# Kernel tuning notes

Measured on AMD Instinct MI355X. Metric: run time of the kernel, lower is better.

## Reference

```python
import jax, jax.numpy as jnp
import numpy as np

B, S, C, V, LAT, NL = 256, 512, 256, 32, 256, 7
DILS = [1, 2, 4, 8, 16, 32, 64]
EPS = 1e-5


def setup_inputs() -> dict:
    key = jax.random.key(0)
    ks = jax.random.split(key, 24)
    s = 0.05
    inp = {
        "x": jax.random.randint(ks[0], (B, S), 0, V, dtype=jnp.int64 if jax.config.read("jax_enable_x64") else jnp.int32),
        "z": jax.random.normal(ks[1], (B, LAT), dtype=jnp.float32),
        "emb": jax.random.normal(ks[2], (V, C), dtype=jnp.float32) * s,
        "latent_W": jax.random.normal(ks[3], (LAT, C), dtype=jnp.float32) * s,
        "latent_b": jnp.zeros((C,), jnp.float32),
        "ln1_g": jnp.ones((NL, C), jnp.float32),
        "ln1_b": jnp.zeros((NL, C), jnp.float32),
        "w1": jax.random.normal(ks[4], (NL, C, C), jnp.float32) * s,
        "b1": jnp.zeros((NL, C), jnp.float32),
        "ln2_g": jnp.ones((NL, C), jnp.float32),
        "ln2_b": jnp.zeros((NL, C), jnp.float32),
        "wd": jax.random.normal(ks[5], (NL, 2, C, C), jnp.float32) * s,  # tap 0 = x[t-d], tap 1 = x[t]
        "bd": jnp.zeros((NL, C), jnp.float32),
        "ln3_g": jnp.ones((NL, C), jnp.float32),
        "ln3_b": jnp.zeros((NL, C), jnp.float32),
        "we": jax.random.normal(ks[6], (NL, C, C), jnp.float32) * s,
        "be": jnp.zeros((NL, C), jnp.float32),
        "wg": jax.random.normal(ks[7], (NL, C, C), jnp.float32) * s,
        "bg": jnp.zeros((NL, C), jnp.float32),
        "out_W": jax.random.normal(ks[8], (C, V), jnp.float32) * s,
        "out_b": jnp.zeros((V,), jnp.float32),
    }
    return inp


def _ln(h, g, b):
    mu = h.mean(-1, keepdims=True)
    var = jnp.mean((h - mu) ** 2, axis=-1, keepdims=True)
    return (h - mu) * jax.lax.rsqrt(var + EPS) * g + b


def _lrelu(h):
    return jnp.where(h >= 0, h, 0.01 * h)


def reference(x, z, emb, latent_W, latent_b, ln1_g, ln1_b, w1, b1,
              ln2_g, ln2_b, wd, bd, ln3_g, ln3_b, we, be, wg, bg,
              out_W, out_b):
    # channel-last layout [B, S, C] throughout (fuses away the torch transposes)
    h = emb[x] + (z @ latent_W + latent_b)[:, None, :]
    for i, d in enumerate(DILS):
        x_inp = h
        t = _lrelu(_ln(x_inp, ln1_g[i], ln1_b[i]))
        t = t @ w1[i] + b1[i]
        t = _lrelu(_ln(t, ln2_g[i], ln2_b[i]))
        # causal dilated conv, kernel=2: out[t] = W0*x[t-d] + W1*x[t]
        t_shift = jnp.pad(t, ((0, 0), (d, 0), (0, 0)))[:, :t.shape[1], :]
        t = t_shift @ wd[i, 0] + t @ wd[i, 1] + bd[i]
        t = _lrelu(_ln(t, ln3_g[i], ln3_b[i]))
        gated = (t @ we[i] + be[i]) * jax.nn.sigmoid(t @ wg[i] + bg[i])
        h = gated + x_inp
    logits = h @ out_W + out_b                      # [B, S, V]
    lp = jax.nn.log_softmax(logits, axis=-1)
    # gather log-prob of next token: lp[:, :-1, :] at x[:, 1:]
    return jnp.take_along_axis(lp[:, :-1, :], x[:, 1:, None], axis=2)[..., 0]
```

## Files before the change

### kernel.cpp

```cpp
#include <hip/hip_runtime.h>

typedef unsigned short u16;
typedef unsigned int   u32;
typedef __attribute__((ext_vector_type(8))) short short8;
typedef __attribute__((ext_vector_type(4))) float f32x4;

struct __align__(8) u16x4 { u16 x, y, z, w; };

#define NL 7
#define M_DIM 131072

__device__ __forceinline__ float b2f(u16 u) {
  union { float f; u32 i; } c; c.i = ((u32)u) << 16; return c.f;
}
__device__ __forceinline__ u16 f2b(float f) {
  union { float f; u32 i; } c; c.f = f;
  u32 r = c.i + 0x7FFFu + ((c.i >> 16) & 1u);
  return (u16)(r >> 16);
}
__device__ __forceinline__ float wave_sum(float v) {
  #pragma unroll
  for (int off = 1; off < 64; off <<= 1) v += __shfl_xor(v, off);
  return v;
}
__device__ __forceinline__ void gload16(const void* g, void* l) {
  __builtin_amdgcn_global_load_lds((const __attribute__((address_space(1))) void*)g,
                                   (__attribute__((address_space(3))) void*)l, 16, 0, 0);
}


__global__ __launch_bounds__(256) void conv_w1_k(const float* __restrict__ w1, u16* __restrict__ wT) {
  int idx = blockIdx.x * 256 + threadIdx.x;
  int i = idx >> 16, rem = idx & 65535;
  int n = rem >> 8, k = rem & 255;
  wT[idx] = f2b(w1[(i << 16) + (k << 8) + n]);
}

__global__ __launch_bounds__(256) void conv_wd_k(const float* __restrict__ wd, u16* __restrict__ wT) {
  int idx = blockIdx.x * 256 + threadIdx.x;
  int i = idx / 131072, rem = idx & 131071;
  int n = rem >> 9, k2 = rem & 511;
  int tap = k2 >> 8, k = k2 & 255;
  wT[idx] = f2b(wd[(((i * 2 + tap) << 8) + k) * 256 + n]);
}

__global__ __launch_bounds__(256) void conv_weg_k(const float* __restrict__ we, const float* __restrict__ wg,
                                                  u16* __restrict__ wT) {
  int idx = blockIdx.x * 256 + threadIdx.x;
  int i = idx / 131072, rem = idx & 131071;
  int src = rem >> 16, n = (rem >> 8) & 255, k = rem & 255;
  const float* W = src ? wg : we;
  wT[idx] = f2b(W[((i << 8) + k) * 256 + n]);
}

__global__ __launch_bounds__(256) void conv_wo_k(const float* __restrict__ outW, u16* __restrict__ wTo) {
  int idx = blockIdx.x * 256 + threadIdx.x;
  int v = idx >> 8, k = idx & 255;
  wTo[idx] = f2b(outW[k * 32 + v]);
}


__global__ __launch_bounds__(256) void zlat_k(const float* __restrict__ z, const float* __restrict__ W,
                                              const float* __restrict__ bias, float* __restrict__ zlat) {
  int b = blockIdx.x, c = threadIdx.x;
  float acc = bias[c];
  for (int l = 0; l < 256; ++l) acc += z[b * 256 + l] * W[l * 256 + c];
  zlat[b * 256 + c] = acc;
}


__device__ __forceinline__ void ln_lrelu4(float v0, float v1, float v2, float v3,
                                          const float* __restrict__ g, const float* __restrict__ b,
                                          int c, u16x4* out) {
  float s = wave_sum(v0 + v1 + v2 + v3);
  float q = wave_sum(v0 * v0 + v1 * v1 + v2 * v2 + v3 * v3);
  float mu = s * 0.00390625f;
  float var = q * 0.00390625f - mu * mu;
  float rs = rsqrtf(var + 1e-5f);
  float4 gv = *(const float4*)&g[c];
  float4 bv = *(const float4*)&b[c];
  float y0 = (v0 - mu) * rs * gv.x + bv.x; y0 = y0 >= 0.f ? y0 : 0.01f * y0;
  float y1 = (v1 - mu) * rs * gv.y + bv.y; y1 = y1 >= 0.f ? y1 : 0.01f * y1;
  float y2 = (v2 - mu) * rs * gv.z + bv.z; y2 = y2 >= 0.f ? y2 : 0.01f * y2;
  float y3 = (v3 - mu) * rs * gv.w + bv.w; y3 = y3 >= 0.f ? y3 : 0.01f * y3;
  out->x = f2b(y0); out->y = f2b(y1); out->z = f2b(y2); out->w = f2b(y3);
}


__global__ __launch_bounds__(256) void embed_ln_k(const int* __restrict__ x, const float* __restrict__ emb,
                                                  const float* __restrict__ zlat,
                                                  const float* __restrict__ g, const float* __restrict__ b,
                                                  u16* __restrict__ h, u16* __restrict__ tOut) {
  int wave = threadIdx.x >> 6, lane = threadIdx.x & 63;
  int r = blockIdx.x * 4 + wave;
  int c = lane * 4;
  int tok = x[r];
  int bi = r >> 9;
  float4 ev = *(const float4*)&emb[tok * 256 + c];
  float4 zv = *(const float4*)&zlat[bi * 256 + c];
  float v0 = ev.x + zv.x, v1 = ev.y + zv.y, v2 = ev.z + zv.z, v3 = ev.w + zv.w;
  u16x4 hb; hb.x = f2b(v0); hb.y = f2b(v1); hb.z = f2b(v2); hb.w = f2b(v3);
  *(u16x4*)&h[(long)r * 256 + c] = hb;
  u16x4 ov;
  ln_lrelu4(v0, v1, v2, v3, g, b, c, &ov);
  *(u16x4*)&tOut[(long)r * 256 + c] = ov;
}


__global__ __launch_bounds__(256) void gemm_ln_k(
    const u16* __restrict__ A, const u16* __restrict__ WT, int Ktot, int dil,
    const float* __restrict__ bias, const float* __restrict__ g, const float* __restrict__ b,
    u16* __restrict__ Out)
{
  __shared__ u16 lA[64 * 32];
  __shared__ u16 lB[256 * 32];
  __shared__ float pS[64][4], pQ[64][4];
  __shared__ float muA[64], rsA[64];
  const int tid = threadIdx.x;
  const int lane = tid & 63;
  const int wv = tid >> 6;
  const int wc = wv * 64;
  const int m0 = blockIdx.x * 64;
  const int rA = tid >> 2;
  const int cA = (tid & 3) * 8;
  const int mm = m0 + rA;
  const int s1 = mm & 511;
  const bool fixBlk = (dil > 0) && ((m0 & 511) < dil);

  f32x4 acc[4][4];
  #pragma unroll
  for (int i = 0; i < 4; ++i)
    #pragma unroll
    for (int j = 0; j < 4; ++j) {
      acc[i][j][0] = 0.f; acc[i][j][1] = 0.f; acc[i][j][2] = 0.f; acc[i][j][3] = 0.f;
    }

  const int nkt = Ktot >> 5;
  for (int kt = 0; kt < nkt; ++kt) {
    const int kk = (kt & 7) * 32;
    int r = mm;
    if (dil > 0 && kt < 8) r = (s1 >= dil) ? (mm - dil) : mm;
    gload16(A + (long)r * 256 + kk + cA, &lA[rA * 32 + cA]);
    const u16* bSrc = WT + (long)rA * Ktot + kt * 32 + cA;
    #pragma unroll
    for (int j = 0; j < 4; ++j)
      gload16(bSrc + (long)(64 * j) * Ktot, &lB[(rA + 64 * j) * 32 + cA]);
    __syncthreads();

    if (fixBlk && kt < 8) {
      if (rA < dil) {
        uint4 zz; zz.x = 0; zz.y = 0; zz.z = 0; zz.w = 0;
        *(uint4*)&lA[rA * 32 + cA] = zz;
      }
      __syncthreads();
    }

    const int lq = (lane >> 4) * 8;
    const int lr = lane & 15;
    short8 af[4], bfr[4];
    #pragma unroll
    for (int mt = 0; mt < 4; ++mt)
      af[mt] = *(const short8*)&lA[(mt * 16 + lr) * 32 + lq];
    #pragma unroll
    for (int nt = 0; nt < 4; ++nt)
      bfr[nt] = *(const short8*)&lB[(wc + nt * 16 + lr) * 32 + lq];
    #pragma unroll
    for (int mt = 0; mt < 4; ++mt)
      #pragma unroll
      for (int nt = 0; nt < 4; ++nt)
        acc[mt][nt] = __builtin_amdgcn_mfma_f32_16x16x32_bf16(af[mt], bfr[nt], acc[mt][nt], 0, 0, 0);
    __syncthreads();
  }

  const int lr = lane & 15;
  const int quad = lane >> 4;
  float biasv[4], gv[4], bv[4];
  #pragma unroll
  for (int nt = 0; nt < 4; ++nt) {
    int n = wc + nt * 16 + lr;
    biasv[nt] = bias[n]; gv[nt] = g[n]; bv[nt] = b[n];
  }
  #pragma unroll
  for (int mt = 0; mt < 4; ++mt)
    #pragma unroll
    for (int r = 0; r < 4; ++r) {
      float s = 0.f, q = 0.f;
      #pragma unroll
      for (int nt = 0; nt < 4; ++nt) {
        float v = acc[mt][nt][r] + biasv[nt];
        acc[mt][nt][r] = v;
        s += v; q += v * v;
      }
      #pragma unroll
      for (int off = 1; off < 16; off <<= 1) {
        s += __shfl_xor(s, off); q += __shfl_xor(q, off);
      }
      if (lr == 0) { pS[mt * 16 + quad * 4 + r][wv] = s; pQ[mt * 16 + quad * 4 + r][wv] = q; }
    }
  __syncthreads();
  if (tid < 64) {
    float S = pS[tid][0] + pS[tid][1] + pS[tid][2] + pS[tid][3];
    float Q = pQ[tid][0] + pQ[tid][1] + pQ[tid][2] + pQ[tid][3];
    float mu = S * 0.00390625f;
    float var = Q * 0.00390625f - mu * mu;
    muA[tid] = mu; rsA[tid] = rsqrtf(var + 1e-5f);
  }
  __syncthreads();
  #pragma unroll
  for (int mt = 0; mt < 4; ++mt)
    #pragma unroll
    for (int r = 0; r < 4; ++r) {
      int row = mt * 16 + quad * 4 + r;
      float mu = muA[row], rs = rsA[row];
      #pragma unroll
      for (int nt = 0; nt < 4; ++nt) {
        float y = (acc[mt][nt][r] - mu) * rs * gv[nt] + bv[nt];
        y = y >= 0.f ? y : 0.01f * y;
        Out[(long)(m0 + row) * 256 + wc + nt * 16 + lr] = f2b(y);
      }
    }
}


__global__ __launch_bounds__(256, 2) void gemm_gate_ln_k(
    const u16* __restrict__ P, const u16* __restrict__ WTe, const u16* __restrict__ WTg,
    const float* __restrict__ be, const float* __restrict__ bg,
    const float* __restrict__ g, const float* __restrict__ b,
    u16* __restrict__ h, u16* __restrict__ tOut, int doLN)
{
  __shared__ u16 lA[64 * 32];
  __shared__ u16 lBe[256 * 32];
  __shared__ u16 lBg[256 * 32];
  __shared__ float pS[64][4], pQ[64][4];
  __shared__ float muA[64], rsA[64];
  const int tid = threadIdx.x;
  const int lane = tid & 63;
  const int wv = tid >> 6;
  const int wc = wv * 64;
  const int m0 = blockIdx.x * 64;
  const int rA = tid >> 2;
  const int cA = (tid & 3) * 8;

  f32x4 accE[4][4], accG[4][4];
  #pragma unroll
  for (int i = 0; i < 4; ++i)
    #pragma unroll
    for (int j = 0; j < 4; ++j) {
      accE[i][j][0] = 0.f; accE[i][j][1] = 0.f; accE[i][j][2] = 0.f; accE[i][j][3] = 0.f;
      accG[i][j][0] = 0.f; accG[i][j][1] = 0.f; accG[i][j][2] = 0.f; accG[i][j][3] = 0.f;
    }

  for (int kt = 0; kt < 8; ++kt) {
    const int kk = kt * 32;
    gload16(P + (long)(m0 + rA) * 256 + kk + cA, &lA[rA * 32 + cA]);
    const long bofs = (long)rA * 256 + kk + cA;
    #pragma unroll
    for (int j = 0; j < 4; ++j) {
      gload16(WTe + bofs + (long)(64 * j) * 256, &lBe[(rA + 64 * j) * 32 + cA]);
      gload16(WTg + bofs + (long)(64 * j) * 256, &lBg[(rA + 64 * j) * 32 + cA]);
    }
    __syncthreads();

    const int lq = (lane >> 4) * 8;
    const int lr = lane & 15;
    short8 af[4], bfe[4], bfg[4];
    #pragma unroll
    for (int mt = 0; mt < 4; ++mt)
      af[mt] = *(const short8*)&lA[(mt * 16 + lr) * 32 + lq];
    #pragma unroll
    for (int nt = 0; nt < 4; ++nt) {
      bfe[nt] = *(const short8*)&lBe[(wc + nt * 16 + lr) * 32 + lq];
      bfg[nt] = *(const short8*)&lBg[(wc + nt * 16 + lr) * 32 + lq];
    }
    #pragma unroll
    for (int mt = 0; mt < 4; ++mt)
      #pragma unroll
      for (int nt = 0; nt < 4; ++nt) {
        accE[mt][nt] = __builtin_amdgcn_mfma_f32_16x16x32_bf16(af[mt], bfe[nt], accE[mt][nt], 0, 0, 0);
        accG[mt][nt] = __builtin_amdgcn_mfma_f32_16x16x32_bf16(af[mt], bfg[nt], accG[mt][nt], 0, 0, 0);
      }
    __syncthreads();
  }

  const int lr = lane & 15;
  const int quad = lane >> 4;
  float bev[4], bgv[4];
  #pragma unroll
  for (int nt = 0; nt < 4; ++nt) {
    int n = wc + nt * 16 + lr;
    bev[nt] = be[n]; bgv[nt] = bg[n];
  }
  #pragma unroll
  for (int mt = 0; mt < 4; ++mt)
    #pragma unroll
    for (int r = 0; r < 4; ++r) {
      int row = mt * 16 + quad * 4 + r;
      long off = (long)(m0 + row) * 256;
      float s = 0.f, q = 0.f;
      #pragma unroll
      for (int nt = 0; nt < 4; ++nt) {
        int n = wc + nt * 16 + lr;
        float e = accE[mt][nt][r] + bev[nt];
        float gg = accG[mt][nt][r] + bgv[nt];
        float hv = b2f(h[off + n]);
        float hn = e * (1.f / (1.f + expf(-gg))) + hv;
        h[off + n] = f2b(hn);
        accE[mt][nt][r] = hn;
        s += hn; q += hn * hn;
      }
      #pragma unroll
      for (int off2 = 1; off2 < 16; off2 <<= 1) {
        s += __shfl_xor(s, off2); q += __shfl_xor(q, off2);
      }
      if (lr == 0) { pS[row][wv] = s; pQ[row][wv] = q; }
    }
  __syncthreads();
  if (tid < 64) {
    float S = pS[tid][0] + pS[tid][1] + pS[tid][2] + pS[tid][3];
    float Q = pQ[tid][0] + pQ[tid][1] + pQ[tid][2] + pQ[tid][3];
    float mu = S * 0.00390625f;
    float var = Q * 0.00390625f - mu * mu;
    muA[tid] = mu; rsA[tid] = rsqrtf(var + 1e-5f);
  }
  __syncthreads();
  if (doLN) {
    float gv[4], bv[4];
    #pragma unroll
    for (int nt = 0; nt < 4; ++nt) {
      int n = wc + nt * 16 + lr;
      gv[nt] = g[n]; bv[nt] = b[n];
    }
    #pragma unroll
    for (int mt = 0; mt < 4; ++mt)
      #pragma unroll
      for (int r = 0; r < 4; ++r) {
        int row = mt * 16 + quad * 4 + r;
        float mu = muA[row], rs = rsA[row];
        #pragma unroll
        for (int nt = 0; nt < 4; ++nt) {
          float y = (accE[mt][nt][r] - mu) * rs * gv[nt] + bv[nt];
          y = y >= 0.f ? y : 0.01f * y;
          tOut[(long)(m0 + row) * 256 + wc + nt * 16 + lr] = f2b(y);
        }
      }
  }
}


__global__ __launch_bounds__(256) void final_k(const u16* __restrict__ h, const u16* __restrict__ WTo,
                                               const float* __restrict__ outb, const int* __restrict__ x,
                                               float* __restrict__ out) {
  __shared__ u16 lW[32 * 264];
  const int tid = threadIdx.x;
  const int lane = tid & 63;
  const int wv = tid >> 6;
  const int mBase = blockIdx.x * 256 + wv * 64;

  #pragma unroll
  for (int j = 0; j < 4; ++j) {
    int chunk = tid + 256 * j;
    int v = chunk >> 5, k8 = chunk & 31;
    uint4 w4 = *(const uint4*)(WTo + v * 256 + k8 * 8);
    *(uint4*)&lW[v * 264 + k8 * 8] = w4;
  }
  __syncthreads();

  const int lq = (lane >> 4) * 8;
  const int lr = lane & 15;
  const int quad = lane >> 4;

  f32x4 acc[4][2];
  #pragma unroll
  for (int mt = 0; mt < 4; ++mt) {
    acc[mt][0][0] = 0.f; acc[mt][0][1] = 0.f; acc[mt][0][2] = 0.f; acc[mt][0][3] = 0.f;
    acc[mt][1][0] = 0.f; acc[mt][1][1] = 0.f; acc[mt][1][2] = 0.f; acc[mt][1][3] = 0.f;
  }

  for (int kt = 0; kt < 8; ++kt) {
    short8 bf0 = *(const short8*)&lW[lr * 264 + kt * 32 + lq];
    short8 bf1 = *(const short8*)&lW[(16 + lr) * 264 + kt * 32 + lq];
    #pragma unroll
    for (int mt = 0; mt < 4; ++mt) {
      short8 af = *(const short8*)(h + (long)(mBase + mt * 16 + lr) * 256 + kt * 32 + lq);
      acc[mt][0] = __builtin_amdgcn_mfma_f32_16x16x32_bf16(af, bf0, acc[mt][0], 0, 0, 0);
      acc[mt][1] = __builtin_amdgcn_mfma_f32_16x16x32_bf16(af, bf1, acc[mt][1], 0, 0, 0);
    }
  }

  float ob0 = outb[lr], ob1 = outb[16 + lr];
  #pragma unroll
  for (int mt = 0; mt < 4; ++mt)
    #pragma unroll
    for (int r = 0; r < 4; ++r) {
      int row = mBase + mt * 16 + quad * 4 + r;
      float lo = acc[mt][0][r] + ob0;
      float hi = acc[mt][1][r] + ob1;
      float mx = fmaxf(lo, hi);
      #pragma unroll
      for (int o = 1; o < 16; o <<= 1) mx = fmaxf(mx, __shfl_xor(mx, o));
      float se = expf(lo - mx) + expf(hi - mx);
      #pragma unroll
      for (int o = 1; o < 16; o <<= 1) se += __shfl_xor(se, o);
      int s = row & 511;
      int xa = (s == 511) ? row : (row + 1);
      int tok = x[xa];
      float lg = (tok < 16) ? lo : hi;
      float lp = lg - mx - logf(se);
      if (s != 511 && lr == (tok & 15))
        out[(row >> 9) * 511 + s] = lp;
    }
}


extern "C" void kernel_launch(void* const* d_in, const int* in_sizes, int n_in,
                              void* d_out, int out_size, void* d_ws, size_t ws_size,
                              hipStream_t stream) {
  const int*   x    = (const int*)d_in[0];
  const float* z    = (const float*)d_in[1];
  const float* emb  = (const float*)d_in[2];
  const float* latW = (const float*)d_in[3];
  const float* latb = (const float*)d_in[4];
  const float* ln1g = (const float*)d_in[5];
  const float* ln1b = (const float*)d_in[6];
  const float* w1   = (const float*)d_in[7];
  const float* b1   = (const float*)d_in[8];
  const float* ln2g = (const float*)d_in[9];
  const float* ln2b = (const float*)d_in[10];
  const float* wd   = (const float*)d_in[11];
  const float* bd   = (const float*)d_in[12];
  const float* ln3g = (const float*)d_in[13];
  const float* ln3b = (const float*)d_in[14];
  const float* we   = (const float*)d_in[15];
  const float* be   = (const float*)d_in[16];
  const float* wg   = (const float*)d_in[17];
  const float* bg   = (const float*)d_in[18];
  const float* outW = (const float*)d_in[19];
  const float* outb = (const float*)d_in[20];

  char* ws = (char*)d_ws;
  u16*   h    = (u16*)(ws + 0);
  u16*   bufA = (u16*)(ws + 67108864);
  u16*   bufB = (u16*)(ws + 134217728);
  float* zlat = (float*)(ws + 201326592);
  u16*   wT1  = (u16*)(ws + 201588736);
  u16*   wTd  = (u16*)(ws + 202506240);
  u16*   wTeg = (u16*)(ws + 204341248);
  u16*   wTo  = (u16*)(ws + 206176256);

  conv_w1_k <<<1792, 256, 0, stream>>>(w1, wT1);
  conv_wd_k <<<3584, 256, 0, stream>>>(wd, wTd);
  conv_weg_k<<<3584, 256, 0, stream>>>(we, wg, wTeg);
  conv_wo_k <<<32, 256, 0, stream>>>(outW, wTo);
  zlat_k    <<<256, 256, 0, stream>>>(z, latW, latb, zlat);
  embed_ln_k<<<M_DIM / 4, 256, 0, stream>>>(x, emb, zlat, ln1g, ln1b, h, bufA);

  u16* X = bufA;
  u16* Y = bufB;
  for (int i = 0; i < NL; ++i) {
    int d = 1 << i;
    int doLN = (i < NL - 1) ? 1 : 0;
    int ni = doLN ? (i + 1) : i;
    gemm_ln_k<<<M_DIM / 64, 256, 0, stream>>>(
        X, wT1 + i * 65536, 256, 0, b1 + i * 256, ln2g + i * 256, ln2b + i * 256, Y);
    gemm_ln_k<<<M_DIM / 64, 256, 0, stream>>>(
        Y, wTd + i * 131072, 512, d, bd + i * 256, ln3g + i * 256, ln3b + i * 256, X);
    gemm_gate_ln_k<<<M_DIM / 64, 256, 0, stream>>>(
        X, wTeg + i * 131072, wTeg + i * 131072 + 65536, be + i * 256, bg + i * 256,
        ln1g + ni * 256, ln1b + ni * 256, h, Y, doLN);
    u16* tmp = X; X = Y; Y = tmp;
  }

  final_k<<<M_DIM / 256, 256, 0, stream>>>(h, wTo, outb, x, (float*)d_out);
}
```

Baseline: 1.693 ms.

## Move LN1 into first GEMM prologue and restage weights through registers

```diff
diff --git a/kernel.cpp b/kernel.cpp
--- a/kernel.cpp
+++ b/kernel.cpp
@@ -17,15 +17,6 @@
   union { float f; u32 i; } c; c.f = f;
   u32 r = c.i + 0x7FFFu + ((c.i >> 16) & 1u);
   return (u16)(r >> 16);
-}
-__device__ __forceinline__ float wave_sum(float v) {
-  #pragma unroll
-  for (int off = 1; off < 64; off <<= 1) v += __shfl_xor(v, off);
-  return v;
-}
-__device__ __forceinline__ void gload16(const void* g, void* l) {
-  __builtin_amdgcn_global_load_lds((const __attribute__((address_space(1))) void*)g,
-                                   (__attribute__((address_space(3))) void*)l, 16, 0, 0);
 }
 
 
@@ -69,28 +60,8 @@
 }
 
 
-__device__ __forceinline__ void ln_lrelu4(float v0, float v1, float v2, float v3,
-                                          const float* __restrict__ g, const float* __restrict__ b,
-                                          int c, u16x4* out) {
-  float s = wave_sum(v0 + v1 + v2 + v3);
-  float q = wave_sum(v0 * v0 + v1 * v1 + v2 * v2 + v3 * v3);
-  float mu = s * 0.00390625f;
-  float var = q * 0.00390625f - mu * mu;
-  float rs = rsqrtf(var + 1e-5f);
-  float4 gv = *(const float4*)&g[c];
-  float4 bv = *(const float4*)&b[c];
-  float y0 = (v0 - mu) * rs * gv.x + bv.x; y0 = y0 >= 0.f ? y0 : 0.01f * y0;
-  float y1 = (v1 - mu) * rs * gv.y + bv.y; y1 = y1 >= 0.f ? y1 : 0.01f * y1;
-  float y2 = (v2 - mu) * rs * gv.z + bv.z; y2 = y2 >= 0.f ? y2 : 0.01f * y2;
-  float y3 = (v3 - mu) * rs * gv.w + bv.w; y3 = y3 >= 0.f ? y3 : 0.01f * y3;
-  out->x = f2b(y0); out->y = f2b(y1); out->z = f2b(y2); out->w = f2b(y3);
-}
-
-
-__global__ __launch_bounds__(256) void embed_ln_k(const int* __restrict__ x, const float* __restrict__ emb,
-                                                  const float* __restrict__ zlat,
-                                                  const float* __restrict__ g, const float* __restrict__ b,
-                                                  u16* __restrict__ h, u16* __restrict__ tOut) {
+__global__ __launch_bounds__(256) void embed_k(const int* __restrict__ x, const float* __restrict__ emb,
+                                               const float* __restrict__ zlat, u16* __restrict__ h) {
   int wave = threadIdx.x >> 6, lane = threadIdx.x & 63;
   int r = blockIdx.x * 4 + wave;
   int c = lane * 4;
@@ -98,34 +69,62 @@
   int bi = r >> 9;
   float4 ev = *(const float4*)&emb[tok * 256 + c];
   float4 zv = *(const float4*)&zlat[bi * 256 + c];
-  float v0 = ev.x + zv.x, v1 = ev.y + zv.y, v2 = ev.z + zv.z, v3 = ev.w + zv.w;
-  u16x4 hb; hb.x = f2b(v0); hb.y = f2b(v1); hb.z = f2b(v2); hb.w = f2b(v3);
+  u16x4 hb;
+  hb.x = f2b(ev.x + zv.x); hb.y = f2b(ev.y + zv.y);
+  hb.z = f2b(ev.z + zv.z); hb.w = f2b(ev.w + zv.w);
   *(u16x4*)&h[(long)r * 256 + c] = hb;
-  u16x4 ov;
-  ln_lrelu4(v0, v1, v2, v3, g, b, c, &ov);
-  *(u16x4*)&tOut[(long)r * 256 + c] = ov;
-}
-
-
-__global__ __launch_bounds__(256) void gemm_ln_k(
-    const u16* __restrict__ A, const u16* __restrict__ WT, int Ktot, int dil,
-    const float* __restrict__ bias, const float* __restrict__ g, const float* __restrict__ b,
-    u16* __restrict__ Out)
+}
+
+
+__global__ __launch_bounds__(256) void gemm1_k(
+    const u16* __restrict__ h, const u16* __restrict__ WT,
+    const float* __restrict__ lnAg, const float* __restrict__ lnAb,
+    const float* __restrict__ bias,
+    const float* __restrict__ lnBg, const float* __restrict__ lnBb,
+    u16* __restrict__ V)
 {
-  __shared__ u16 lA[64 * 32];
-  __shared__ u16 lB[256 * 32];
-  __shared__ float pS[64][4], pQ[64][4];
-  __shared__ float muA[64], rsA[64];
+  __shared__ __align__(16) u16 sm[64 * 264 + 256 * 40];
+  u16* lA = sm;
+  u16* lB = sm + 64 * 264;
   const int tid = threadIdx.x;
   const int lane = tid & 63;
   const int wv = tid >> 6;
   const int wc = wv * 64;
   const int m0 = blockIdx.x * 64;
-  const int rA = tid >> 2;
-  const int cA = (tid & 3) * 8;
-  const int mm = m0 + rA;
-  const int s1 = mm & 511;
-  const bool fixBlk = (dil > 0) && ((m0 & 511) < dil);
+  const int lr = lane & 15;
+  const int quad = lane >> 4;
+  const int lq = quad * 8;
+  const int rB = tid >> 2;
+  const int cB = tid & 3;
+
+  uint4 bq0 = *(const uint4*)(WT + (long)rB * 256 + cB * 8);
+  uint4 bq1 = *(const uint4*)(WT + (long)(rB + 64) * 256 + cB * 8);
+  uint4 bq2 = *(const uint4*)(WT + (long)(rB + 128) * 256 + cB * 8);
+  uint4 bq3 = *(const uint4*)(WT + (long)(rB + 192) * 256 + cB * 8);
+
+  {
+    float4 gv = *(const float4*)&lnAg[lane * 4];
+    float4 bv = *(const float4*)&lnAb[lane * 4];
+    #pragma unroll 4
+    for (int it = 0; it < 16; ++it) {
+      int row = wv * 16 + it;
+      u16x4 hv = *(const u16x4*)&h[(long)(m0 + row) * 256 + lane * 4];
+      float v0 = b2f(hv.x), v1 = b2f(hv.y), v2 = b2f(hv.z), v3 = b2f(hv.w);
+      float s = v0 + v1 + v2 + v3;
+      float q = v0 * v0 + v1 * v1 + v2 * v2 + v3 * v3;
+      #pragma unroll
+      for (int o = 1; o < 64; o <<= 1) { s += __shfl_xor(s, o); q += __shfl_xor(q, o); }
+      float mu = s * 0.00390625f;
+      float var = q * 0.00390625f - mu * mu;
+      float rs = rsqrtf(var + 1e-5f);
+      float y0 = (v0 - mu) * rs * gv.x + bv.x; y0 = y0 >= 0.f ? y0 : 0.01f * y0;
+      float y1 = (v1 - mu) * rs * gv.y + bv.y; y1 = y1 >= 0.f ? y1 : 0.01f * y1;
+      float y2 = (v2 - mu) * rs * gv.z + bv.z; y2 = y2 >= 0.f ? y2 : 0.01f * y2;
+      float y3 = (v3 - mu) * rs * gv.w + bv.w; y3 = y3 >= 0.f ? y3 : 0.01f * y3;
+      u16x4 ov; ov.x = f2b(y0); ov.y = f2b(y1); ov.z = f2b(y2); ov.w = f2b(y3);
+      *(u16x4*)&lA[row * 264 + lane * 4] = ov;
+    }
+  }
 
   f32x4 acc[4][4];
   #pragma unroll
@@ -135,50 +134,45 @@
       acc[i][j][0] = 0.f; acc[i][j][1] = 0.f; acc[i][j][2] = 0.f; acc[i][j][3] = 0.f;
     }
 
-  const int nkt = Ktot >> 5;
-  for (int kt = 0; kt < nkt; ++kt) {
-    const int kk = (kt & 7) * 32;
-    int r = mm;
-    if (dil > 0 && kt < 8) r = (s1 >= dil) ? (mm - dil) : mm;
-    gload16(A + (long)r * 256 + kk + cA, &lA[rA * 32 + cA]);
-    const u16* bSrc = WT + (long)rA * Ktot + kt * 32 + cA;
-    #pragma unroll
-    for (int j = 0; j < 4; ++j)
-      gload16(bSrc + (long)(64 * j) * Ktot, &lB[(rA + 64 * j) * 32 + cA]);
+  for (int kt = 0; kt < 8; ++kt) {
     __syncthreads();
-
-    if (fixBlk && kt < 8) {
-      if (rA < dil) {
-        uint4 zz; zz.x = 0; zz.y = 0; zz.z = 0; zz.w = 0;
-        *(uint4*)&lA[rA * 32 + cA] = zz;
-      }
-      __syncthreads();
-    }
-
-    const int lq = (lane >> 4) * 8;
-    const int lr = lane & 15;
+    *(uint4*)&lB[rB * 40 + cB * 8] = bq0;
+    *(uint4*)&lB[(rB + 64) * 40 + cB * 8] = bq1;
+    *(uint4*)&lB[(rB + 128) * 40 + cB * 8] = bq2;
+    *(uint4*)&lB[(rB + 192) * 40 + cB * 8] = bq3;
+    __syncthreads();
+    if (kt < 7) {
+      const u16* src = WT + (kt + 1) * 32 + cB * 8;
+      bq0 = *(const uint4*)(src + (long)rB * 256);
+      bq1 = *(const uint4*)(src + (long)(rB + 64) * 256);
+      bq2 = *(const uint4*)(src + (long)(rB + 128) * 256);
+      bq3 = *(const uint4*)(src + (long)(rB + 192) * 256);
+    }
     short8 af[4], bfr[4];
     #pragma unroll
     for (int mt = 0; mt < 4; ++mt)
-      af[mt] = *(const short8*)&lA[(mt * 16 + lr) * 32 + lq];
+      af[mt] = *(const short8*)&lA[(mt * 16 + lr) * 264 + kt * 32 + lq];
     #pragma unroll
     for (int nt = 0; nt < 4; ++nt)
-      bfr[nt] = *(const short8*)&lB[(wc + nt * 16 + lr) * 32 + lq];
+      bfr[nt] = *(const short8*)&lB[(wc + nt * 16 + lr) * 40 + lq];
     #pragma unroll
     for (int mt = 0; mt < 4; ++mt)
       #pragma unroll
       for (int nt = 0; nt < 4; ++nt)
         acc[mt][nt] = __builtin_amdgcn_mfma_f32_16x16x32_bf16(af[mt], bfr[nt], acc[mt][nt], 0, 0, 0);
-    __syncthreads();
-  }
-
-  const int lr = lane & 15;
-  const int quad = lane >> 4;
-  float biasv[4], gv[4], bv[4];
+  }
+  __syncthreads();
+
+  float* pS  = (float*)sm;
+  float* pQ  = pS + 256;
+  float* muA = pQ + 256;
+  float* rsA = muA + 64;
+
+  float biasv[4], gv2[4], bv2[4];
   #pragma unroll
   for (int nt = 0; nt < 4; ++nt) {
     int n = wc + nt * 16 + lr;
-    biasv[nt] = bias[n]; gv[nt] = g[n]; bv[nt] = b[n];
+    biasv[nt] = bias[n]; gv2[nt] = lnBg[n]; bv2[nt] = lnBb[n];
   }
   #pragma unroll
   for (int mt = 0; mt < 4; ++mt)
@@ -192,15 +186,16 @@
         s += v; q += v * v;
       }
       #pragma unroll
-      for (int off = 1; off < 16; off <<= 1) {
-        s += __shfl_xor(s, off); q += __shfl_xor(q, off);
-      }
-      if (lr == 0) { pS[mt * 16 + quad * 4 + r][wv] = s; pQ[mt * 16 + quad * 4 + r][wv] = q; }
+      for (int o = 1; o < 16; o <<= 1) { s += __shfl_xor(s, o); q += __shfl_xor(q, o); }
+      if (lr == 0) {
+        int row = mt * 16 + quad * 4 + r;
+        pS[row * 4 + wv] = s; pQ[row * 4 + wv] = q;
+      }
     }
   __syncthreads();
   if (tid < 64) {
-    float S = pS[tid][0] + pS[tid][1] + pS[tid][2] + pS[tid][3];
-    float Q = pQ[tid][0] + pQ[tid][1] + pQ[tid][2] + pQ[tid][3];
+    float S = pS[tid * 4] + pS[tid * 4 + 1] + pS[tid * 4 + 2] + pS[tid * 4 + 3];
+    float Q = pQ[tid * 4] + pQ[tid * 4 + 1] + pQ[tid * 4 + 2] + pQ[tid * 4 + 3];
     float mu = S * 0.00390625f;
     float var = Q * 0.00390625f - mu * mu;
     muA[tid] = mu; rsA[tid] = rsqrtf(var + 1e-5f);
@@ -214,32 +209,156 @@
       float mu = muA[row], rs = rsA[row];
       #pragma unroll
       for (int nt = 0; nt < 4; ++nt) {
-        float y = (acc[mt][nt][r] - mu) * rs * gv[nt] + bv[nt];
+        float y = (acc[mt][nt][r] - mu) * rs * gv2[nt] + bv2[nt];
         y = y >= 0.f ? y : 0.01f * y;
-        Out[(long)(m0 + row) * 256 + wc + nt * 16 + lr] = f2b(y);
-      }
-    }
-}
-
-
-__global__ __launch_bounds__(256, 2) void gemm_gate_ln_k(
-    const u16* __restrict__ P, const u16* __restrict__ WTe, const u16* __restrict__ WTg,
-    const float* __restrict__ be, const float* __restrict__ bg,
-    const float* __restrict__ g, const float* __restrict__ b,
-    u16* __restrict__ h, u16* __restrict__ tOut, int doLN)
+        V[(long)(m0 + row) * 256 + wc + nt * 16 + lr] = f2b(y);
+      }
+    }
+}
+
+
+__global__ __launch_bounds__(256) void dil_k(
+    const u16* __restrict__ V, const u16* __restrict__ WT, int dil,
+    const float* __restrict__ bias, const float* __restrict__ lng, const float* __restrict__ lnb,
+    u16* __restrict__ P)
 {
-  __shared__ u16 lA[64 * 32];
-  __shared__ u16 lBe[256 * 32];
-  __shared__ u16 lBg[256 * 32];
-  __shared__ float pS[64][4], pQ[64][4];
-  __shared__ float muA[64], rsA[64];
+  __shared__ __align__(16) u16 lB[256 * 40];
+  __shared__ float pS[256], pQ[256], muA[64], rsA[64];
   const int tid = threadIdx.x;
   const int lane = tid & 63;
   const int wv = tid >> 6;
   const int wc = wv * 64;
   const int m0 = blockIdx.x * 64;
-  const int rA = tid >> 2;
-  const int cA = (tid & 3) * 8;
+  const int lr = lane & 15;
+  const int quad = lane >> 4;
+  const int lq = quad * 8;
+  const int rB = tid >> 2;
+  const int cB = tid & 3;
+
+  uint4 bq0 = *(const uint4*)(WT + (long)rB * 512 + cB * 8);
+  uint4 bq1 = *(const uint4*)(WT + (long)(rB + 64) * 512 + cB * 8);
+  uint4 bq2 = *(const uint4*)(WT + (long)(rB + 128) * 512 + cB * 8);
+  uint4 bq3 = *(const uint4*)(WT + (long)(rB + 192) * 512 + cB * 8);
+
+  f32x4 acc[4][4];
+  #pragma unroll
+  for (int i = 0; i < 4; ++i)
+    #pragma unroll
+    for (int j = 0; j < 4; ++j) {
+      acc[i][j][0] = 0.f; acc[i][j][1] = 0.f; acc[i][j][2] = 0.f; acc[i][j][3] = 0.f;
+    }
+
+  const short8 zfrag = {0, 0, 0, 0, 0, 0, 0, 0};
+  for (int kt = 0; kt < 16; ++kt) {
+    const int kk = (kt & 7) * 32;
+    const bool tap0 = (kt < 8);
+    short8 af[4];
+    #pragma unroll
+    for (int mt = 0; mt < 4; ++mt) {
+      int m = m0 + mt * 16 + lr;
+      int s = m & 511;
+      int r = (tap0 && s >= dil) ? (m - dil) : m;
+      af[mt] = *(const short8*)(V + (long)r * 256 + kk + lq);
+      if (tap0 && s < dil) af[mt] = zfrag;
+    }
+    __syncthreads();
+    *(uint4*)&lB[rB * 40 + cB * 8] = bq0;
+    *(uint4*)&lB[(rB + 64) * 40 + cB * 8] = bq1;
+    *(uint4*)&lB[(rB + 128) * 40 + cB * 8] = bq2;
+    *(uint4*)&lB[(rB + 192) * 40 + cB * 8] = bq3;
+    __syncthreads();
+    if (kt < 15) {
+      const u16* src = WT + (kt + 1) * 32 + cB * 8;
+      bq0 = *(const uint4*)(src + (long)rB * 512);
+      bq1 = *(const uint4*)(src + (long)(rB + 64) * 512);
+      bq2 = *(const uint4*)(src + (long)(rB + 128) * 512);
+      bq3 = *(const uint4*)(src + (long)(rB + 192) * 512);
+    }
+    short8 bfr[4];
+    #pragma unroll
+    for (int nt = 0; nt < 4; ++nt)
+      bfr[nt] = *(const short8*)&lB[(wc + nt * 16 + lr) * 40 + lq];
+    #pragma unroll
+    for (int mt = 0; mt < 4; ++mt)
+      #pragma unroll
+      for (int nt = 0; nt < 4; ++nt)
+        acc[mt][nt] = __builtin_amdgcn_mfma_f32_16x16x32_bf16(af[mt], bfr[nt], acc[mt][nt], 0, 0, 0);
+  }
+
+  float biasv[4], gv2[4], bv2[4];
+  #pragma unroll
+  for (int nt = 0; nt < 4; ++nt) {
+    int n = wc + nt * 16 + lr;
+    biasv[nt] = bias[n]; gv2[nt] = lng[n]; bv2[nt] = lnb[n];
+  }
+  #pragma unroll
+  for (int mt = 0; mt < 4; ++mt)
+    #pragma unroll
+    for (int r = 0; r < 4; ++r) {
+      float s = 0.f, q = 0.f;
+      #pragma unroll
+      for (int nt = 0; nt < 4; ++nt) {
+        float v = acc[mt][nt][r] + biasv[nt];
+        acc[mt][nt][r] = v;
+        s += v; q += v * v;
+      }
+      #pragma unroll
+      for (int o = 1; o < 16; o <<= 1) { s += __shfl_xor(s, o); q += __shfl_xor(q, o); }
+      if (lr == 0) {
+        int row = mt * 16 + quad * 4 + r;
+        pS[row * 4 + wv] = s; pQ[row * 4 + wv] = q;
+      }
+    }
+  __syncthreads();
+  if (tid < 64) {
+    float S = pS[tid * 4] + pS[tid * 4 + 1] + pS[tid * 4 + 2] + pS[tid * 4 + 3];
+    float Q = pQ[tid * 4] + pQ[tid * 4 + 1] + pQ[tid * 4 + 2] + pQ[tid * 4 + 3];
+    float mu = S * 0.00390625f;
+    float var = Q * 0.00390625f - mu * mu;
+    muA[tid] = mu; rsA[tid] = rsqrtf(var + 1e-5f);
+  }
+  __syncthreads();
+  #pragma unroll
+  for (int mt = 0; mt < 4; ++mt)
+    #pragma unroll
+    for (int r = 0; r < 4; ++r) {
+      int row = mt * 16 + quad * 4 + r;
+      float mu = muA[row], rs = rsA[row];
+      #pragma unroll
+      for (int nt = 0; nt < 4; ++nt) {
+        float y = (acc[mt][nt][r] - mu) * rs * gv2[nt] + bv2[nt];
+        y = y >= 0.f ? y : 0.01f * y;
+        P[(long)(m0 + row) * 256 + wc + nt * 16 + lr] = f2b(y);
+      }
+    }
+}
+
+
+__global__ __launch_bounds__(256, 2) void gate_k(
+    const u16* __restrict__ P, const u16* __restrict__ WTe, const u16* __restrict__ WTg,
+    const float* __restrict__ be, const float* __restrict__ bg, u16* __restrict__ h)
+{
+  __shared__ __align__(16) u16 lBe[256 * 40];
+  __shared__ __align__(16) u16 lBg[256 * 40];
+  const int tid = threadIdx.x;
+  const int lane = tid & 63;
+  const int wv = tid >> 6;
+  const int wc = wv * 64;
+  const int m0 = blockIdx.x * 64;
+  const int lr = lane & 15;
+  const int quad = lane >> 4;
+  const int lq = quad * 8;
+  const int rB = tid >> 2;
+  const int cB = tid & 3;
+
+  uint4 be0 = *(const uint4*)(WTe + (long)rB * 256 + cB * 8);
+  uint4 be1 = *(const uint4*)(WTe + (long)(rB + 64) * 256 + cB * 8);
+  uint4 be2 = *(const uint4*)(WTe + (long)(rB + 128) * 256 + cB * 8);
+  uint4 be3 = *(const uint4*)(WTe + (long)(rB + 192) * 256 + cB * 8);
+  uint4 bg0 = *(const uint4*)(WTg + (long)rB * 256 + cB * 8);
+  uint4 bg1 = *(const uint4*)(WTg + (long)(rB + 64) * 256 + cB * 8);
+  uint4 bg2 = *(const uint4*)(WTg + (long)(rB + 128) * 256 + cB * 8);
+  uint4 bg3 = *(const uint4*)(WTg + (long)(rB + 192) * 256 + cB * 8);
 
   f32x4 accE[4][4], accG[4][4];
   #pragma unroll
@@ -252,25 +371,37 @@
 
   for (int kt = 0; kt < 8; ++kt) {
     const int kk = kt * 32;
-    gload16(P + (long)(m0 + rA) * 256 + kk + cA, &lA[rA * 32 + cA]);
-    const long bofs = (long)rA * 256 + kk + cA;
-    #pragma unroll
-    for (int j = 0; j < 4; ++j) {
-      gload16(WTe + bofs + (long)(64 * j) * 256, &lBe[(rA + 64 * j) * 32 + cA]);
-      gload16(WTg + bofs + (long)(64 * j) * 256, &lBg[(rA + 64 * j) * 32 + cA]);
-    }
+    short8 af[4];
+    #pragma unroll
+    for (int mt = 0; mt < 4; ++mt)
+      af[mt] = *(const short8*)(P + (long)(m0 + mt * 16 + lr) * 256 + kk + lq);
     __syncthreads();
-
-    const int lq = (lane >> 4) * 8;
-    const int lr = lane & 15;
-    short8 af[4], bfe[4], bfg[4];
-    #pragma unroll
-    for (int mt = 0; mt < 4; ++mt)
-      af[mt] = *(const short8*)&lA[(mt * 16 + lr) * 32 + lq];
+    *(uint4*)&lBe[rB * 40 + cB * 8] = be0;
+    *(uint4*)&lBe[(rB + 64) * 40 + cB * 8] = be1;
+    *(uint4*)&lBe[(rB + 128) * 40 + cB * 8] = be2;
+    *(uint4*)&lBe[(rB + 192) * 40 + cB * 8] = be3;
+    *(uint4*)&lBg[rB * 40 + cB * 8] = bg0;
+    *(uint4*)&lBg[(rB + 64) * 40 + cB * 8] = bg1;
+    *(uint4*)&lBg[(rB + 128) * 40 + cB * 8] = bg2;
+    *(uint4*)&lBg[(rB + 192) * 40 + cB * 8] = bg3;
+    __syncthreads();
+    if (kt < 7) {
+      const u16* se = WTe + (kt + 1) * 32 + cB * 8;
+      const u16* sg = WTg + (kt + 1) * 32 + cB * 8;
+      be0 = *(const uint4*)(se + (long)rB * 256);
+      be1 = *(const uint4*)(se + (long)(rB + 64) * 256);
+      be2 = *(const uint4*)(se + (long)(rB + 128) * 256);
+      be3 = *(const uint4*)(se + (long)(rB + 192) * 256);
+      bg0 = *(const uint4*)(sg + (long)rB * 256);
+      bg1 = *(const uint4*)(sg + (long)(rB + 64) * 256);
+      bg2 = *(const uint4*)(sg + (long)(rB + 128) * 256);
+      bg3 = *(const uint4*)(sg + (long)(rB + 192) * 256);
+    }
+    short8 bfe[4], bfg[4];
     #pragma unroll
     for (int nt = 0; nt < 4; ++nt) {
-      bfe[nt] = *(const short8*)&lBe[(wc + nt * 16 + lr) * 32 + lq];
-      bfg[nt] = *(const short8*)&lBg[(wc + nt * 16 + lr) * 32 + lq];
+      bfe[nt] = *(const short8*)&lBe[(wc + nt * 16 + lr) * 40 + lq];
+      bfg[nt] = *(const short8*)&lBg[(wc + nt * 16 + lr) * 40 + lq];
     }
     #pragma unroll
     for (int mt = 0; mt < 4; ++mt)
@@ -279,11 +410,8 @@
         accE[mt][nt] = __builtin_amdgcn_mfma_f32_16x16x32_bf16(af[mt], bfe[nt], accE[mt][nt], 0, 0, 0);
         accG[mt][nt] = __builtin_amdgcn_mfma_f32_16x16x32_bf16(af[mt], bfg[nt], accG[mt][nt], 0, 0, 0);
       }
-    __syncthreads();
-  }
-
-  const int lr = lane & 15;
-  const int quad = lane >> 4;
+  }
+
   float bev[4], bgv[4];
   #pragma unroll
   for (int nt = 0; nt < 4; ++nt) {
@@ -296,54 +424,16 @@
     for (int r = 0; r < 4; ++r) {
       int row = mt * 16 + quad * 4 + r;
       long off = (long)(m0 + row) * 256;
-      float s = 0.f, q = 0.f;
       #pragma unroll
       for (int nt = 0; nt < 4; ++nt) {
         int n = wc + nt * 16 + lr;
         float e = accE[mt][nt][r] + bev[nt];
-        float gg = accG[mt][nt][r] + bgv[nt];
+        float g = accG[mt][nt][r] + bgv[nt];
         float hv = b2f(h[off + n]);
-        float hn = e * (1.f / (1.f + expf(-gg))) + hv;
+        float hn = e * (1.f / (1.f + expf(-g))) + hv;
         h[off + n] = f2b(hn);
-        accE[mt][nt][r] = hn;
-        s += hn; q += hn * hn;
-      }
-      #pragma unroll
-      for (int off2 = 1; off2 < 16; off2 <<= 1) {
-        s += __shfl_xor(s, off2); q += __shfl_xor(q, off2);
-      }
-      if (lr == 0) { pS[row][wv] = s; pQ[row][wv] = q; }
-    }
-  __syncthreads();
-  if (tid < 64) {
-    float S = pS[tid][0] + pS[tid][1] + pS[tid][2] + pS[tid][3];
-    float Q = pQ[tid][0] + pQ[tid][1] + pQ[tid][2] + pQ[tid][3];
-    float mu = S * 0.00390625f;
-    float var = Q * 0.00390625f - mu * mu;
-    muA[tid] = mu; rsA[tid] = rsqrtf(var + 1e-5f);
-  }
-  __syncthreads();
-  if (doLN) {
-    float gv[4], bv[4];
-    #pragma unroll
-    for (int nt = 0; nt < 4; ++nt) {
-      int n = wc + nt * 16 + lr;
-      gv[nt] = g[n]; bv[nt] = b[n];
-    }
-    #pragma unroll
-    for (int mt = 0; mt < 4; ++mt)
-      #pragma unroll
-      for (int r = 0; r < 4; ++r) {
-        int row = mt * 16 + quad * 4 + r;
-        float mu = muA[row], rs = rsA[row];
-        #pragma unroll
-        for (int nt = 0; nt < 4; ++nt) {
-          float y = (accE[mt][nt][r] - mu) * rs * gv[nt] + bv[nt];
-          y = y >= 0.f ? y : 0.01f * y;
-          tOut[(long)(m0 + row) * 256 + wc + nt * 16 + lr] = f2b(y);
-        }
-      }
-  }
+      }
+    }
 }
 
 
@@ -439,8 +529,8 @@
 
   char* ws = (char*)d_ws;
   u16*   h    = (u16*)(ws + 0);
-  u16*   bufA = (u16*)(ws + 67108864);
-  u16*   bufB = (u16*)(ws + 134217728);
+  u16*   v    = (u16*)(ws + 67108864);
+  u16*   p    = (u16*)(ws + 134217728);
   float* zlat = (float*)(ws + 201326592);
   u16*   wT1  = (u16*)(ws + 201588736);
   u16*   wTd  = (u16*)(ws + 202506240);
@@ -452,22 +542,17 @@
   conv_weg_k<<<3584, 256, 0, stream>>>(we, wg, wTeg);
   conv_wo_k <<<32, 256, 0, stream>>>(outW, wTo);
   zlat_k    <<<256, 256, 0, stream>>>(z, latW, latb, zlat);
-  embed_ln_k<<<M_DIM / 4, 256, 0, stream>>>(x, emb, zlat, ln1g, ln1b, h, bufA);
-
-  u16* X = bufA;
-  u16* Y = bufB;
+  embed_k   <<<M_DIM / 4, 256, 0, stream>>>(x, emb, zlat, h);
+
   for (int i = 0; i < NL; ++i) {
     int d = 1 << i;
-    int doLN = (i < NL - 1) ? 1 : 0;
-    int ni = doLN ? (i + 1) : i;
-    gemm_ln_k<<<M_DIM / 64, 256, 0, stream>>>(
-        X, wT1 + i * 65536, 256, 0, b1 + i * 256, ln2g + i * 256, ln2b + i * 256, Y);
-    gemm_ln_k<<<M_DIM / 64, 256, 0, stream>>>(
-        Y, wTd + i * 131072, 512, d, bd + i * 256, ln3g + i * 256, ln3b + i * 256, X);
-    gemm_gate_ln_k<<<M_DIM / 64, 256, 0, stream>>>(
-        X, wTeg + i * 131072, wTeg + i * 131072 + 65536, be + i * 256, bg + i * 256,
-        ln1g + ni * 256, ln1b + ni * 256, h, Y, doLN);
-    u16* tmp = X; X = Y; Y = tmp;
+    gemm1_k<<<M_DIM / 64, 256, 0, stream>>>(
+        h, wT1 + i * 65536, ln1g + i * 256, ln1b + i * 256, b1 + i * 256,
+        ln2g + i * 256, ln2b + i * 256, v);
+    dil_k<<<M_DIM / 64, 256, 0, stream>>>(
+        v, wTd + i * 131072, d, bd + i * 256, ln3g + i * 256, ln3b + i * 256, p);
+    gate_k<<<M_DIM / 64, 256, 0, stream>>>(
+        p, wTeg + i * 131072, wTeg + i * 131072 + 65536, be + i * 256, bg + i * 256, h);
   }
 
   final_k<<<M_DIM / 256, 256, 0, stream>>>(h, wTo, outb, x, (float*)d_out);
```

Result: slower. 1.914 ms (+13.1%).
